# Performance work log

Measured on AMD Instinct MI355X. Metric: run time of the kernel, lower is better.

Reference implementation:

```python
import jax, jax.numpy as jnp
import numpy as np

GAMMA = -0.1   # l0_gamma
ZETA = 1.1     # l0_zeta
BETA = 0.66    # l0_beta (hard-concrete temperature)
LAMBDA = 0.01  # lambda_reg (post-warmup current_lambda)
EPS = 1e-12


def _layernorm(x, g, b, eps=1e-5):
    mu = jnp.mean(x, axis=-1, keepdims=True)
    var = jnp.var(x, axis=-1, keepdims=True)
    return (x - mu) / jnp.sqrt(var + eps) * g + b


def setup_inputs() -> dict:
    key = jax.random.key(0)
    ks = jax.random.split(key, 12)
    B, N, D, H, E, C = 8, 512, 512, 256, 32, 2
    node_feat = jax.random.normal(ks[0], (B, N, D), jnp.float32)
    labels = jax.random.randint(ks[1], (B,), 0, C)
    a = (jax.random.uniform(ks[2], (B, N, N)) < 0.05).astype(jnp.float32)
    adjs = jnp.maximum(a, jnp.swapaxes(a, 1, 2)) * (1.0 - jnp.eye(N, dtype=jnp.float32))
    masks = jnp.ones((B, N), jnp.float32)
    init = lambda k, shp, fan: jax.random.normal(k, shp, jnp.float32) / np.sqrt(fan).astype(np.float32)
    return {
        "node_feat": node_feat, "labels": labels, "adjs": adjs, "masks": masks,
        # edge scorer MLP: concat([h_i,h_j]) -> edge_dim -> 1, factorized as Wa@h_i + Wb@h_j
        "Wa": init(ks[3], (D, E), D), "Wb": init(ks[4], (D, E), D), "be": jnp.zeros((E,), jnp.float32),
        "W2e": init(ks[5], (E, 1), E), "b2e": jnp.zeros((1,), jnp.float32),
        # conv: Linear(feature_dim, hidden_dim)
        "Wconv": init(ks[6], (D, H), D), "bconv": jnp.zeros((H,), jnp.float32),
        # classifier: Linear(H,H//2) -> ReLU -> LayerNorm -> spectral_norm(Linear(H//2,C))
        "W1c": init(ks[7], (H, H // 2), H), "b1c": jnp.zeros((H // 2,), jnp.float32),
        "ln_g": jnp.ones((H // 2,), jnp.float32), "ln_b": jnp.zeros((H // 2,), jnp.float32),
        "W2c": init(ks[8], (H // 2, C), H // 2), "b2c": jnp.zeros((C,), jnp.float32),
        "u_sn": jax.random.normal(ks[9], (C,), jnp.float32),  # spectral-norm power-iteration buffer
    }


def reference(node_feat, labels, adjs, masks, Wa, Wb, be, W2e, b2e,
              Wconv, bconv, W1c, b1c, ln_g, ln_b, W2c, b2c, u_sn):
    B = node_feat.shape[0]
    # F.normalize(node_feat, p=2, dim=2)
    nrm = jnp.sqrt(jnp.sum(node_feat * node_feat, axis=2, keepdims=True))
    nf = node_feat / jnp.maximum(nrm, EPS)
    # edge scoring: logAlpha[b,i,j] = MLP([h_i ; h_j])
    e1 = nf @ Wa                                  # [B,N,E]
    e2 = nf @ Wb                                  # [B,N,E]
    hpair = jax.nn.relu(e1[:, :, None, :] + e2[:, None, :, :] + be)   # [B,N,N,E]
    logAlpha = jnp.einsum('bije,e->bij', hpair, W2e[:, 0]) + b2e[0]    # [B,N,N]
    # deterministic hard-concrete gate (eval mode): clip(sigmoid(logAlpha)*(zeta-gamma)+gamma, 0, 1)
    gate = jnp.clip(jax.nn.sigmoid(logAlpha) * (ZETA - GAMMA) + GAMMA, 0.0, 1.0)
    edge_weights = gate * adjs
    # aggregate: row-normalized weighted adjacency
    wadj = adjs * edge_weights
    row_sum = jnp.sum(wadj, axis=2, keepdims=True) + 1e-8
    h = jnp.einsum('bij,bjd->bid', wadj / row_sum, nf)
    h = jax.nn.relu(h @ Wconv + bconv)            # [B,N,H]
    # edge-weighted attention pooling: node importance = weighted degree, masked softmax
    imp = jnp.sum(wadj, axis=2)                    # [B,N]
    attn_logits = jnp.where(masks > 0, imp, -1e9)
    attn = jax.nn.softmax(attn_logits, axis=1)
    graph_rep = jnp.einsum('bn,bnh->bh', attn, h)  # [B,H]
    # classifier
    z = jax.nn.relu(graph_rep @ W1c + b1c)
    z = _layernorm(z, ln_g, ln_b)
    # spectral norm (1 power iteration, u/v stop-gradded like torch buffers)
    v = W2c @ u_sn
    v = jax.lax.stop_gradient(v / jnp.maximum(jnp.linalg.norm(v), EPS))
    u2 = W2c.T @ v
    u2 = jax.lax.stop_gradient(u2 / jnp.maximum(jnp.linalg.norm(u2), EPS))
    sigma = v @ (W2c @ u2)
    logits = z @ (W2c / sigma) + b2c              # [B,C]
    # losses
    logp = jax.nn.log_softmax(logits, axis=1)
    cls_loss = -jnp.mean(logp[jnp.arange(B), labels])
    l0_penalty = jnp.sum(jax.nn.sigmoid(logAlpha - BETA * jnp.log(-GAMMA / ZETA)))
    total_loss = cls_loss + LAMBDA * l0_penalty
    return logits, total_loss, adjs * edge_weights
```

## Files before the change

### kernel.cpp

```cpp
#include <hip/hip_runtime.h>


#define Bsz 8
#define Nn  512
#define Dd  512
#define Hh  256
#define Ee  32

#define WS_NFPK   0L
#define WS_E1     1048576L
#define WS_E2     1179648L
#define WS_WADJB  1310720L
#define WS_RS     1835008L
#define WS_L0     1839104L
#define WS_HAGGB  1839112L
#define WS_H      2363400L
#define WS_GR     3411976L

typedef __bf16 bf16x8 __attribute__((ext_vector_type(8)));
typedef float  f32x4  __attribute__((ext_vector_type(4)));

__device__ inline ushort f2bf(float f) {
  union { float f; unsigned u; } c; c.f = f;
  return (ushort)((c.u + 0x7fffu + ((c.u >> 16) & 1u)) >> 16);
}

__global__ __launch_bounds__(256) void norm_e12_fused(
    const float* __restrict__ nfeat, const float* __restrict__ Wa,
    const float* __restrict__ Wb, const float* __restrict__ be,
    ushort* __restrict__ nfpk, float* __restrict__ e1, float* __restrict__ e2,
    float* __restrict__ row_sum, float* __restrict__ gr,
    float* __restrict__ l0_sum)
{
  const int blk = blockIdx.x;
  const int r0 = blk*16;
  const int b = r0 >> 9;
  const int t = threadIdx.x;
  const int r = t >> 4;
  const int seg = t & 15;

  __shared__ ushort As[(63*17 + 15 + 1)*8];
  __shared__ ushort Bs[4*64*8];

  float4 v[8];
  const float* src = nfeat + (long)(r0 + r)*Dd + seg*32;
  #pragma unroll
  for (int i = 0; i < 8; ++i) v[i] = *(const float4*)(src + i*4);
  float s = 0.f;
  #pragma unroll
  for (int i = 0; i < 8; ++i)
    s += v[i].x*v[i].x + v[i].y*v[i].y + v[i].z*v[i].z + v[i].w*v[i].w;
  #pragma unroll
  for (int m = 1; m < 16; m <<= 1) s += __shfl_xor(s, m, 16);
  const float sc = 1.f / fmaxf(sqrtf(s), 1e-12f);
  #pragma unroll
  for (int q = 0; q < 4; ++q) {
    ushort tmp[8];
    const float4 a = v[2*q], bq = v[2*q+1];
    tmp[0]=f2bf(a.x*sc);  tmp[1]=f2bf(a.y*sc);  tmp[2]=f2bf(a.z*sc);  tmp[3]=f2bf(a.w*sc);
    tmp[4]=f2bf(bq.x*sc); tmp[5]=f2bf(bq.y*sc); tmp[6]=f2bf(bq.z*sc); tmp[7]=f2bf(bq.w*sc);
    *(uint4*)(As + ((seg*4 + q)*17 + r)*8) = *(uint4*)tmp;
  }
  if (t < 16) row_sum[r0 + t] = 0.f;
  if (blk == 0) {
    for (int p = t; p < Bsz*Hh; p += 256) gr[p] = 0.f;
    if (t == 0) *l0_sum = 0.f;
  }
  __syncthreads();

  #pragma unroll
  for (int p = 0; p < 4; ++p) {
    const int g = t + p*256;
    const int oct = g >> 9, d = g & 511;
    ushort tmp[8];
    #pragma unroll
    for (int j = 0; j < 8; ++j)
      tmp[j] = As[((d >> 3)*17 + oct*8 + j)*8 + (d & 7)];
    const long og = ((r0 & 511) >> 3) + oct;
    *(uint4*)(nfpk + ((long)b*262144 + (og*512 + d)*8)) = *(uint4*)tmp;
  }

  const int lane = t & 63, l15 = lane & 15, quad = lane >> 4;
  const int w = t >> 6;
  f32x4 acc = {0.f, 0.f, 0.f, 0.f};
  const int bn = t & 63, bkq = t >> 6;
  for (int k0 = 0; k0 < 512; k0 += 32) {
    ushort tmp[8];
    {
      const float* W = (bn < 32) ? Wa : Wb;
      const int col = bn & 31;
      #pragma unroll
      for (int j = 0; j < 8; ++j)
        tmp[j] = f2bf(W[(long)(k0 + bkq*8 + j)*Ee + col]);
    }
    __syncthreads();
    *(uint4*)(Bs + (bkq*64 + bn)*8) = *(uint4*)tmp;
    __syncthreads();
    const bf16x8 af  = *(const bf16x8*)(As + (((k0 >> 3) + quad)*17 + l15)*8);
    const bf16x8 bfr = *(const bf16x8*)(Bs + (quad*64 + w*16 + l15)*8);
    acc = __builtin_amdgcn_mfma_f32_16x16x32_bf16(af, bfr, acc, 0, 0, 0);
  }
  const int col = w*16 + l15;
  #pragma unroll
  for (int rr = 0; rr < 4; ++rr) {
    const int row = r0 + quad*4 + rr;
    if (col < 32) e1[(long)row*Ee + col] = acc[rr] + be[col];
    else          e2[(long)row*Ee + (col - 32)] = acc[rr];
  }
}

__global__ __launch_bounds__(256) void edge_kernel(
    const float* __restrict__ e1, const float* __restrict__ e2,
    const float* __restrict__ W2e, const float* __restrict__ b2e,
    const float* __restrict__ adjs, float* __restrict__ out_wadj,
    ushort* __restrict__ wadj_b, float* __restrict__ row_sum,
    float* __restrict__ l0_sum)
{
  const int b  = blockIdx.z;
  const int i0 = blockIdx.y * 32;
  const int j0 = blockIdx.x * 128;
  const int t  = threadIdx.x;

  __shared__ float e2s[32*132];

  #pragma unroll
  for (int itr = 0; itr < 4; ++itr) {
    const int idx = t + itr*256;
    const int kq = idx & 7, jg = idx >> 3;
    const float4 v = *(const float4*)(e2 + ((long)(b*Nn + j0 + jg))*Ee + kq*4);
    e2s[(kq*4+0)*132 + jg] = v.x;
    e2s[(kq*4+1)*132 + jg] = v.y;
    e2s[(kq*4+2)*132 + jg] = v.z;
    e2s[(kq*4+3)*132 + jg] = v.w;
  }

  const int pair  = t >> 4;
  const int jslot = t & 15;
  const int ia = i0 + pair*2;
  const int ib = ia + 1;
  const int ja = jslot*4;
  const int jb = ja + 64;

  float e1af[32], e1bf[32], w2f[32];
  #pragma unroll
  for (int q = 0; q < 8; ++q) {
    *(float4*)(&e1af[q*4]) = *(const float4*)(e1 + ((long)(b*Nn + ia))*Ee + q*4);
    *(float4*)(&e1bf[q*4]) = *(const float4*)(e1 + ((long)(b*Nn + ib))*Ee + q*4);
    *(float4*)(&w2f[q*4])  = *(const float4*)(W2e + q*4);
  }
  const float b2 = b2e[0];
  __syncthreads();

  float acc[2][8] = {};
  #pragma unroll
  for (int k = 0; k < 32; ++k) {
    const float4 va = *(const float4*)(e2s + k*132 + ja);
    const float4 vb = *(const float4*)(e2s + k*132 + jb);
    const float w = w2f[k];
    const float ea = e1af[k], eb = e1bf[k];
    acc[0][0] += fmaxf(ea+va.x, 0.f)*w;
    acc[0][1] += fmaxf(ea+va.y, 0.f)*w;
    acc[0][2] += fmaxf(ea+va.z, 0.f)*w;
    acc[0][3] += fmaxf(ea+va.w, 0.f)*w;
    acc[0][4] += fmaxf(ea+vb.x, 0.f)*w;
    acc[0][5] += fmaxf(ea+vb.y, 0.f)*w;
    acc[0][6] += fmaxf(ea+vb.z, 0.f)*w;
    acc[0][7] += fmaxf(ea+vb.w, 0.f)*w;
    acc[1][0] += fmaxf(eb+va.x, 0.f)*w;
    acc[1][1] += fmaxf(eb+va.y, 0.f)*w;
    acc[1][2] += fmaxf(eb+va.z, 0.f)*w;
    acc[1][3] += fmaxf(eb+va.w, 0.f)*w;
    acc[1][4] += fmaxf(eb+vb.x, 0.f)*w;
    acc[1][5] += fmaxf(eb+vb.y, 0.f)*w;
    acc[1][6] += fmaxf(eb+vb.z, 0.f)*w;
    acc[1][7] += fmaxf(eb+vb.w, 0.f)*w;
  }

  float rs[2] = {0.f, 0.f};
  float l0acc = 0.f;
  #pragma unroll
  for (int ii = 0; ii < 2; ++ii) {
    const int i = (ii == 0) ? ia : ib;
    const float* arow = adjs     + ((long)(b*Nn + i))*Nn + j0;
    ushort* bwrow     = wadj_b   + ((long)(b*Nn + i))*Nn + j0;
    float* outrow     = out_wadj + ((long)(b*Nn + i))*Nn + j0;
    #pragma unroll
    for (int h2 = 0; h2 < 2; ++h2) {
      const int jl = (h2 == 0) ? ja : jb;
      const float4 av = *(const float4*)(arow + jl);
      float wv[4];
      #pragma unroll
      for (int c = 0; c < 4; ++c) {
        const float logA = acc[ii][h2*4 + c] + b2;
        const float sg = 1.f/(1.f + expf(-logA));
        const float gate = fminf(fmaxf(sg*1.2f - 0.1f, 0.f), 1.f);
        const float a = (c==0)?av.x:(c==1)?av.y:(c==2)?av.z:av.w;
        const float w = gate*a*a;
        wv[c] = w;
        rs[ii] += w;
        l0acc += 1.f/(1.f + expf(-(logA + 1.58261088f)));
      }
      ushort4 bw;
      bw.x = f2bf(wv[0]); bw.y = f2bf(wv[1]); bw.z = f2bf(wv[2]); bw.w = f2bf(wv[3]);
      *(ushort4*)(bwrow + jl) = bw;
      outrow[jl+0] = wv[0]; outrow[jl+1] = wv[1];
      outrow[jl+2] = wv[2]; outrow[jl+3] = wv[3];
    }
  }

  #pragma unroll
  for (int m = 1; m < 16; m <<= 1) {
    rs[0] += __shfl_xor(rs[0], m, 16);
    rs[1] += __shfl_xor(rs[1], m, 16);
  }
  if (jslot == 0) {
    atomicAdd(&row_sum[b*Nn + ia], rs[0]);
    atomicAdd(&row_sum[b*Nn + ib], rs[1]);
  }
  #pragma unroll
  for (int m = 1; m < 64; m <<= 1) l0acc += __shfl_xor(l0acc, m, 64);
  if ((t & 63) == 0) atomicAdd(l0_sum, l0acc);
}

template<int OP>
__global__ __launch_bounds__(256) void mfma_gemm64(
    const ushort* __restrict__ A, const ushort* __restrict__ Bpk,
    const float* __restrict__ Bf32, int M, int N, int K,
    long sA, long sB, long sC, const float* __restrict__ aux,
    ushort* __restrict__ Cb, float* __restrict__ Cf)
{
  const int bb = blockIdx.z;
  const int m0 = blockIdx.y*64, n0 = blockIdx.x*64;
  const int t = threadIdx.x;
  const int lane = t & 63, l15 = lane & 15, quad = lane >> 4;
  const int wv = t >> 6, wr = wv & 1, wc = wv >> 1;

  __shared__ ushort As[(3*65 + 63 + 1)*8];
  __shared__ ushort Bs[4*64*8];

  const ushort* Ab = A + (long)bb*sA;
  const int am = t >> 2, akq = t & 3;
  const int bn = t & 63, bkq = t >> 6;

  f32x4 acc[2][2];
  #pragma unroll
  for (int i = 0; i < 2; ++i)
    #pragma unroll
    for (int j = 0; j < 2; ++j) acc[i][j] = (f32x4){0.f,0.f,0.f,0.f};

  uint4 ra = *(const uint4*)(Ab + (long)(m0+am)*K + akq*8);
  uint4 rbu;
  float rbf[8];
  if (OP == 0) {
    const ushort* Bb = Bpk + (long)bb*sB;
    rbu = *(const uint4*)(Bb + ((long)bkq*N + n0 + bn)*8);
  } else {
    #pragma unroll
    for (int j = 0; j < 8; ++j) rbf[j] = Bf32[(long)(bkq*8 + j)*N + n0 + bn];
  }

  for (int k0 = 0; k0 < K; k0 += 32) {
    *(uint4*)(As + (akq*65 + am)*8) = ra;
    if (OP == 0) {
      *(uint4*)(Bs + (bkq*64 + bn)*8) = rbu;
    } else {
      ushort tmp[8];
      #pragma unroll
      for (int j = 0; j < 8; ++j) tmp[j] = f2bf(rbf[j]);
      *(uint4*)(Bs + (bkq*64 + bn)*8) = *(uint4*)tmp;
    }
    __syncthreads();
    if (k0 + 32 < K) {
      ra = *(const uint4*)(Ab + (long)(m0+am)*K + (k0+32) + akq*8);
      if (OP == 0) {
        const ushort* Bb = Bpk + (long)bb*sB;
        rbu = *(const uint4*)(Bb + ((long)(((k0+32) >> 3) + bkq)*N + n0 + bn)*8);
      } else {
        #pragma unroll
        for (int j = 0; j < 8; ++j)
          rbf[j] = Bf32[(long)(k0 + 32 + bkq*8 + j)*N + n0 + bn];
      }
    }
    bf16x8 af[2], bfr[2];
    #pragma unroll
    for (int i = 0; i < 2; ++i)
      af[i] = *(const bf16x8*)(As + (quad*65 + wr*32 + i*16 + l15)*8);
    #pragma unroll
    for (int j = 0; j < 2; ++j)
      bfr[j] = *(const bf16x8*)(Bs + (quad*64 + wc*32 + j*16 + l15)*8);
    #pragma unroll
    for (int i = 0; i < 2; ++i)
      #pragma unroll
      for (int j = 0; j < 2; ++j)
        acc[i][j] = __builtin_amdgcn_mfma_f32_16x16x32_bf16(
            af[i], bfr[j], acc[i][j], 0, 0, 0);
    __syncthreads();
  }

  #pragma unroll
  for (int i = 0; i < 2; ++i) {
    #pragma unroll
    for (int j = 0; j < 2; ++j) {
      const int col = n0 + wc*32 + j*16 + l15;
      #pragma unroll
      for (int rr = 0; rr < 4; ++rr) {
        const int row = m0 + wr*32 + i*16 + quad*4 + rr;
        float v2 = acc[i][j][rr];
        if (OP == 0) {
          const float scl = 1.f/(aux[bb*M + row] + 1e-8f);
          Cb[(long)bb*sC + (long)row*N + col] = f2bf(v2*scl);
        } else {
          v2 += aux[col];
          Cf[(long)row*N + col] = fmaxf(v2, 0.f);
        }
      }
    }
  }
}

__global__ __launch_bounds__(256) void pool_fused(
    const float* __restrict__ row_sum, const float* __restrict__ masks,
    const float* __restrict__ h, float* __restrict__ gr)
{
  const int ic = blockIdx.x, b = blockIdx.y;
  const int t = threadIdx.x;
  __shared__ float red[256];
  __shared__ float attn_s[64];
  const float m0 = masks[b*Nn + t], m1 = masks[b*Nn + t + 256];
  const float l0v = (m0 > 0.f) ? row_sum[b*Nn + t] : -1e9f;
  const float l1v = (m1 > 0.f) ? row_sum[b*Nn + t + 256] : -1e9f;
  red[t] = fmaxf(l0v, l1v); __syncthreads();
  for (int s = 128; s > 0; s >>= 1) { if (t < s) red[t] = fmaxf(red[t], red[t+s]); __syncthreads(); }
  const float mx = red[0]; __syncthreads();
  const float ev0 = expf(l0v - mx), ev1 = expf(l1v - mx);
  red[t] = ev0 + ev1; __syncthreads();
  for (int s = 128; s > 0; s >>= 1) { if (t < s) red[t] += red[t+s]; __syncthreads(); }
  const float sinv = 1.f/red[0];
  __syncthreads();
  if (t < 64) {
    const int node = ic*64 + t;
    const float mm = masks[b*Nn + node];
    const float lv = (mm > 0.f) ? row_sum[b*Nn + node] : -1e9f;
    attn_s[t] = expf(lv - mx)*sinv;
  }
  __syncthreads();
  float acc = 0.f;
  #pragma unroll 4
  for (int i2 = 0; i2 < 64; ++i2)
    acc += attn_s[i2]*h[((long)(b*Nn + ic*64 + i2))*Hh + t];
  atomicAdd(&gr[b*Hh + t], acc);
}

__global__ __launch_bounds__(256) void classifier_kernel(
    const float* __restrict__ gr, const float* __restrict__ W1c,
    const float* __restrict__ b1c, const float* __restrict__ ln_g,
    const float* __restrict__ ln_b, const float* __restrict__ W2c,
    const float* __restrict__ b2c, const float* __restrict__ u_sn,
    const int* __restrict__ labels, const float* __restrict__ l0_sum,
    float* __restrict__ out)
{
  const int t = threadIdx.x;
  __shared__ float grs[2048];
  __shared__ float z[8][128];
  __shared__ float red[256];
  __shared__ float vv[128];
  __shared__ float mu_s[8], ri_s[8];
  __shared__ float lg[16];
  for (int p = t; p < 2048; p += 256) grs[p] = gr[p];
  __syncthreads();
  #pragma unroll
  for (int p = 0; p < 4; ++p) {
    const int idx = t + p*256;
    const int b = idx >> 7, o = idx & 127;
    float acc = b1c[o];
    for (int d = 0; d < 256; ++d) acc += grs[b*256 + d]*W1c[d*128 + o];
    z[b][o] = fmaxf(acc, 0.f);
  }
  __syncthreads();
  if (t < 8) {
    float mu = 0.f;
    for (int o = 0; o < 128; ++o) mu += z[t][o];
    mu *= (1.f/128.f);
    float var = 0.f;
    for (int o = 0; o < 128; ++o) { const float d = z[t][o]-mu; var += d*d; }
    var *= (1.f/128.f);
    mu_s[t] = mu; ri_s[t] = rsqrtf(var + 1e-5f);
  }
  const float u0 = u_sn[0], u1 = u_sn[1];
  float vt = 0.f;
  if (t < 128) { vt = W2c[2*t]*u0 + W2c[2*t+1]*u1; vv[t] = vt; }
  red[t] = (t < 128) ? vt*vt : 0.f;
  __syncthreads();
  for (int s = 128; s > 0; s >>= 1) { if (t < s) red[t] += red[t+s]; __syncthreads(); }
  const float vninv = 1.f/fmaxf(sqrtf(red[0]), 1e-12f);
  __syncthreads();
  red[t] = (t < 128) ? W2c[2*t]*vv[t]*vninv : 0.f;
  __syncthreads();
  for (int s = 128; s > 0; s >>= 1) { if (t < s) red[t] += red[t+s]; __syncthreads(); }
  const float u20 = red[0];
  __syncthreads();
  red[t] = (t < 128) ? W2c[2*t+1]*vv[t]*vninv : 0.f;
  __syncthreads();
  for (int s = 128; s > 0; s >>= 1) { if (t < s) red[t] += red[t+s]; __syncthreads(); }
  const float u21 = red[0];
  __syncthreads();
  const float uninv = 1.f/fmaxf(sqrtf(u20*u20 + u21*u21), 1e-12f);
  const float u2n0 = u20*uninv, u2n1 = u21*uninv;
  red[t] = (t < 128) ? vv[t]*vninv*(W2c[2*t]*u2n0 + W2c[2*t+1]*u2n1) : 0.f;
  __syncthreads();
  for (int s = 128; s > 0; s >>= 1) { if (t < s) red[t] += red[t+s]; __syncthreads(); }
  const float sinv = 1.f/red[0];
  __syncthreads();
  if (t < 16) {
    const int b = t >> 1, c = t & 1;
    const float mu = mu_s[b], ri = ri_s[b];
    float acc = 0.f;
    for (int o = 0; o < 128; ++o) {
      const float zln = (z[b][o]-mu)*ri*ln_g[o] + ln_b[o];
      acc += zln*W2c[2*o + c];
    }
    const float lgv = acc*sinv + b2c[c];
    lg[t] = lgv;
    out[t] = lgv;
  }
  __syncthreads();
  if (t == 0) {
    float closs = 0.f;
    for (int b = 0; b < 8; ++b) {
      const float a0 = lg[2*b], a1 = lg[2*b+1];
      const float m = fmaxf(a0, a1);
      const float lse = m + logf(expf(a0-m) + expf(a1-m));
      closs += lse - lg[2*b + labels[b]];
    }
    closs *= (1.f/8.f);
    out[16] = closs + 0.01f*l0_sum[0];
  }
}

extern "C" void kernel_launch(void* const* d_in, const int* in_sizes, int n_in,
                              void* d_out, int out_size, void* d_ws, size_t ws_size,
                              hipStream_t stream) {
  const float* node_feat = (const float*)d_in[0];
  const int*   labels    = (const int*)d_in[1];
  const float* adjs      = (const float*)d_in[2];
  const float* masks     = (const float*)d_in[3];
  const float* Wa        = (const float*)d_in[4];
  const float* Wb        = (const float*)d_in[5];
  const float* be        = (const float*)d_in[6];
  const float* W2e       = (const float*)d_in[7];
  const float* b2e       = (const float*)d_in[8];
  const float* Wconv     = (const float*)d_in[9];
  const float* bconv     = (const float*)d_in[10];
  const float* W1c       = (const float*)d_in[11];
  const float* b1c       = (const float*)d_in[12];
  const float* ln_g      = (const float*)d_in[13];
  const float* ln_b      = (const float*)d_in[14];
  const float* W2c       = (const float*)d_in[15];
  const float* b2c       = (const float*)d_in[16];
  const float* u_sn      = (const float*)d_in[17];

  float* out = (float*)d_out;
  float* ws  = (float*)d_ws;
  ushort* nfpk   = (ushort*)(ws + WS_NFPK);
  float*  e1     = ws + WS_E1;
  float*  e2     = ws + WS_E2;
  ushort* wadjb  = (ushort*)(ws + WS_WADJB);
  float*  row_sum= ws + WS_RS;
  float*  l0s    = ws + WS_L0;
  ushort* haggb  = (ushort*)(ws + WS_HAGGB);
  float*  h      = ws + WS_H;
  float*  gr     = ws + WS_GR;

  norm_e12_fused<<<256, 256, 0, stream>>>(node_feat, Wa, Wb, be, nfpk, e1, e2,
                                          row_sum, gr, l0s);
  edge_kernel<<<dim3(Nn/128, Nn/32, Bsz), 256, 0, stream>>>(
      e1, e2, W2e, b2e, adjs, out + 17, wadjb, row_sum, l0s);
  mfma_gemm64<0><<<dim3(8, 8, 8), 256, 0, stream>>>(
      wadjb, nfpk, nullptr, 512, 512, 512, 262144L, 262144L, 262144L,
      row_sum, haggb, nullptr);
  mfma_gemm64<1><<<dim3(4, 64, 1), 256, 0, stream>>>(
      haggb, nullptr, Wconv, 4096, 256, 512, 0, 0, 0,
      bconv, nullptr, h);
  pool_fused<<<dim3(8, Bsz), 256, 0, stream>>>(row_sum, masks, h, gr);
  classifier_kernel<<<1, 256, 0, stream>>>(gr, W1c, b1c, ln_g, ln_b, W2c, b2c,
                                           u_sn, labels, l0s, out);
}
```

Measured before the change: 201.8 us.

## Reassociate conv GEMM before aggregation and fuse aggregation with attention pooling

```diff
diff --git a/kernel.cpp b/kernel.cpp
--- a/kernel.cpp
+++ b/kernel.cpp
@@ -7,15 +7,15 @@
 #define Hh  256
 #define Ee  32
 
-#define WS_NFPK   0L
-#define WS_E1     1048576L
-#define WS_E2     1179648L
-#define WS_WADJB  1310720L
+#define WS_NFCPK  0L
+#define WS_E1     524288L
+#define WS_E2     655360L
+#define WS_WADJB  786432L
 #define WS_RS     1835008L
 #define WS_L0     1839104L
-#define WS_HAGGB  1839112L
-#define WS_H      2363400L
-#define WS_GR     3411976L
+#define WS_GR     1839112L
+#define WS_WABPK  1841160L
+#define WS_WCPK   1857544L
 
 typedef __bf16 bf16x8 __attribute__((ext_vector_type(8)));
 typedef float  f32x4  __attribute__((ext_vector_type(4)));
@@ -25,10 +25,34 @@
   return (ushort)((c.u + 0x7fffu + ((c.u >> 16) & 1u)) >> 16);
 }
 
-__global__ __launch_bounds__(256) void norm_e12_fused(
-    const float* __restrict__ nfeat, const float* __restrict__ Wa,
-    const float* __restrict__ Wb, const float* __restrict__ be,
-    ushort* __restrict__ nfpk, float* __restrict__ e1, float* __restrict__ e2,
+__global__ __launch_bounds__(256) void pack_weights(
+    const float* __restrict__ Wconv, const float* __restrict__ Wa,
+    const float* __restrict__ Wb, ushort* __restrict__ wcpk,
+    ushort* __restrict__ wabpk)
+{
+  const int g = blockIdx.x*256 + threadIdx.x;
+  if (g < 16384) {
+    const int kq = g >> 8, n = g & 255;
+    ushort tmp[8];
+    #pragma unroll
+    for (int j = 0; j < 8; ++j) tmp[j] = f2bf(Wconv[(kq*8 + j)*Hh + n]);
+    *(uint4*)(wcpk + (long)g*8) = *(uint4*)tmp;
+  } else if (g < 16384 + 4096) {
+    const int gg = g - 16384;
+    const int kq = gg >> 6, n = gg & 63;
+    const float* W = (n < 32) ? Wa : Wb;
+    const int e = n & 31;
+    ushort tmp[8];
+    #pragma unroll
+    for (int j = 0; j < 8; ++j) tmp[j] = f2bf(W[(kq*8 + j)*Ee + e]);
+    *(uint4*)(wabpk + (long)gg*8) = *(uint4*)tmp;
+  }
+}
+
+__global__ __launch_bounds__(256) void norm_e12_nfc(
+    const float* __restrict__ nfeat, const ushort* __restrict__ wabpk,
+    const ushort* __restrict__ wcpk, const float* __restrict__ be,
+    ushort* __restrict__ nfcpk, float* __restrict__ e1, float* __restrict__ e2,
     float* __restrict__ row_sum, float* __restrict__ gr,
     float* __restrict__ l0_sum)
 {
@@ -40,7 +64,8 @@
   const int seg = t & 15;
 
   __shared__ ushort As[(63*17 + 15 + 1)*8];
-  __shared__ ushort Bs[4*64*8];
+  __shared__ ushort BsA[4*64*8];
+  __shared__ ushort BsC[4*256*8];
 
   float4 v[8];
   const float* src = nfeat + (long)(r0 + r)*Dd + seg*32;
@@ -66,46 +91,82 @@
     for (int p = t; p < Bsz*Hh; p += 256) gr[p] = 0.f;
     if (t == 0) *l0_sum = 0.f;
   }
-  __syncthreads();
-
+
+  const int lane = t & 63, l15 = lane & 15, quad = lane >> 4;
+  const int w = t >> 6;
+  const int abq = t >> 6, abn = t & 63;
+
+  f32x4 acc_e = {0.f, 0.f, 0.f, 0.f};
+  f32x4 acc_c[4];
+  #pragma unroll
+  for (int j = 0; j < 4; ++j) acc_c[j] = (f32x4){0.f,0.f,0.f,0.f};
+
+  uint4 pab = *(const uint4*)(wabpk + ((long)abq*64 + abn)*8);
+  uint4 pc[4];
   #pragma unroll
   for (int p = 0; p < 4; ++p) {
     const int g = t + p*256;
-    const int oct = g >> 9, d = g & 511;
+    pc[p] = *(const uint4*)(wcpk + ((long)(g >> 8)*256 + (g & 255))*8);
+  }
+  __syncthreads();
+
+  for (int k0 = 0; k0 < 512; k0 += 32) {
+    if (k0 > 0) __syncthreads();
+    *(uint4*)(BsA + (abq*64 + abn)*8) = pab;
+    #pragma unroll
+    for (int p = 0; p < 4; ++p) {
+      const int g = t + p*256;
+      *(uint4*)(BsC + ((g >> 8)*256 + (g & 255))*8) = pc[p];
+    }
+    __syncthreads();
+    if (k0 + 32 < 512) {
+      const int kb = (k0 + 32) >> 3;
+      pab = *(const uint4*)(wabpk + ((long)(kb + abq)*64 + abn)*8);
+      #pragma unroll
+      for (int p = 0; p < 4; ++p) {
+        const int g = t + p*256;
+        pc[p] = *(const uint4*)(wcpk + ((long)(kb + (g >> 8))*256 + (g & 255))*8);
+      }
+    }
+    const bf16x8 af = *(const bf16x8*)(As + (((k0 >> 3) + quad)*17 + l15)*8);
+    const bf16x8 bfa = *(const bf16x8*)(BsA + (quad*64 + w*16 + l15)*8);
+    acc_e = __builtin_amdgcn_mfma_f32_16x16x32_bf16(af, bfa, acc_e, 0, 0, 0);
+    #pragma unroll
+    for (int fn = 0; fn < 4; ++fn) {
+      const bf16x8 bfc = *(const bf16x8*)(BsC + (quad*256 + w*64 + fn*16 + l15)*8);
+      acc_c[fn] = __builtin_amdgcn_mfma_f32_16x16x32_bf16(af, bfc, acc_c[fn], 0, 0, 0);
+    }
+  }
+
+  {
+    const int col = w*16 + l15;
+    #pragma unroll
+    for (int rr = 0; rr < 4; ++rr) {
+      const int row = r0 + quad*4 + rr;
+      if (col < 32) e1[(long)row*Ee + col] = acc_e[rr] + be[col];
+      else          e2[(long)row*Ee + (col - 32)] = acc_e[rr];
+    }
+  }
+
+  __syncthreads();
+  ushort* tile = BsC;
+  #pragma unroll
+  for (int fn = 0; fn < 4; ++fn) {
+    const int col = w*64 + fn*16 + l15;
+    #pragma unroll
+    for (int rr = 0; rr < 4; ++rr)
+      tile[(quad*4 + rr)*260 + col] = f2bf(acc_c[fn][rr]);
+  }
+  __syncthreads();
+  #pragma unroll
+  for (int p = 0; p < 2; ++p) {
+    const int g = t + p*256;
+    const int oct = g >> 8, c = g & 255;
     ushort tmp[8];
     #pragma unroll
-    for (int j = 0; j < 8; ++j)
-      tmp[j] = As[((d >> 3)*17 + oct*8 + j)*8 + (d & 7)];
+    for (int j = 0; j < 8; ++j) tmp[j] = tile[(oct*8 + j)*260 + c];
     const long og = ((r0 & 511) >> 3) + oct;
-    *(uint4*)(nfpk + ((long)b*262144 + (og*512 + d)*8)) = *(uint4*)tmp;
-  }
-
-  const int lane = t & 63, l15 = lane & 15, quad = lane >> 4;
-  const int w = t >> 6;
-  f32x4 acc = {0.f, 0.f, 0.f, 0.f};
-  const int bn = t & 63, bkq = t >> 6;
-  for (int k0 = 0; k0 < 512; k0 += 32) {
-    ushort tmp[8];
-    {
-      const float* W = (bn < 32) ? Wa : Wb;
-      const int col = bn & 31;
-      #pragma unroll
-      for (int j = 0; j < 8; ++j)
-        tmp[j] = f2bf(W[(long)(k0 + bkq*8 + j)*Ee + col]);
-    }
-    __syncthreads();
-    *(uint4*)(Bs + (bkq*64 + bn)*8) = *(uint4*)tmp;
-    __syncthreads();
-    const bf16x8 af  = *(const bf16x8*)(As + (((k0 >> 3) + quad)*17 + l15)*8);
-    const bf16x8 bfr = *(const bf16x8*)(Bs + (quad*64 + w*16 + l15)*8);
-    acc = __builtin_amdgcn_mfma_f32_16x16x32_bf16(af, bfr, acc, 0, 0, 0);
-  }
-  const int col = w*16 + l15;
-  #pragma unroll
-  for (int rr = 0; rr < 4; ++rr) {
-    const int row = r0 + quad*4 + rr;
-    if (col < 32) e1[(long)row*Ee + col] = acc[rr] + be[col];
-    else          e2[(long)row*Ee + (col - 32)] = acc[rr];
+    *(uint4*)(nfcpk + ((long)b*16384 + og*256 + c)*8) = *(uint4*)tmp;
   }
 }
 
@@ -222,12 +283,10 @@
   if ((t & 63) == 0) atomicAdd(l0_sum, l0acc);
 }
 
-template<int OP>
-__global__ __launch_bounds__(256) void mfma_gemm64(
-    const ushort* __restrict__ A, const ushort* __restrict__ Bpk,
-    const float* __restrict__ Bf32, int M, int N, int K,
-    long sA, long sB, long sC, const float* __restrict__ aux,
-    ushort* __restrict__ Cb, float* __restrict__ Cf)
+__global__ __launch_bounds__(256) void gemm_pool(
+    const ushort* __restrict__ wadjb, const ushort* __restrict__ nfcpk,
+    const float* __restrict__ row_sum, const float* __restrict__ masks,
+    const float* __restrict__ bconv, float* __restrict__ gr)
 {
   const int bb = blockIdx.z;
   const int m0 = blockIdx.y*64, n0 = blockIdx.x*64;
@@ -237,8 +296,13 @@
 
   __shared__ ushort As[(3*65 + 63 + 1)*8];
   __shared__ ushort Bs[4*64*8];
-
-  const ushort* Ab = A + (long)bb*sA;
+  __shared__ float ptile[64*65];
+  __shared__ float red[256];
+  __shared__ float attn_s[64];
+  __shared__ float mx_s, sinv_s;
+
+  const ushort* Ab = wadjb + (long)bb*262144;
+  const ushort* Bb = nfcpk + (long)bb*131072;
   const int am = t >> 2, akq = t & 3;
   const int bn = t & 63, bkq = t >> 6;
 
@@ -248,38 +312,17 @@
     #pragma unroll
     for (int j = 0; j < 2; ++j) acc[i][j] = (f32x4){0.f,0.f,0.f,0.f};
 
-  uint4 ra = *(const uint4*)(Ab + (long)(m0+am)*K + akq*8);
-  uint4 rbu;
-  float rbf[8];
-  if (OP == 0) {
-    const ushort* Bb = Bpk + (long)bb*sB;
-    rbu = *(const uint4*)(Bb + ((long)bkq*N + n0 + bn)*8);
-  } else {
-    #pragma unroll
-    for (int j = 0; j < 8; ++j) rbf[j] = Bf32[(long)(bkq*8 + j)*N + n0 + bn];
-  }
-
-  for (int k0 = 0; k0 < K; k0 += 32) {
+  uint4 ra = *(const uint4*)(Ab + (long)(m0+am)*512 + akq*8);
+  uint4 rb = *(const uint4*)(Bb + ((long)bkq*256 + n0 + bn)*8);
+
+  for (int k0 = 0; k0 < 512; k0 += 32) {
+    if (k0 > 0) __syncthreads();
     *(uint4*)(As + (akq*65 + am)*8) = ra;
-    if (OP == 0) {
-      *(uint4*)(Bs + (bkq*64 + bn)*8) = rbu;
-    } else {
-      ushort tmp[8];
-      #pragma unroll
-      for (int j = 0; j < 8; ++j) tmp[j] = f2bf(rbf[j]);
-      *(uint4*)(Bs + (bkq*64 + bn)*8) = *(uint4*)tmp;
-    }
+    *(uint4*)(Bs + (bkq*64 + bn)*8) = rb;
     __syncthreads();
-    if (k0 + 32 < K) {
-      ra = *(const uint4*)(Ab + (long)(m0+am)*K + (k0+32) + akq*8);
-      if (OP == 0) {
-        const ushort* Bb = Bpk + (long)bb*sB;
-        rbu = *(const uint4*)(Bb + ((long)(((k0+32) >> 3) + bkq)*N + n0 + bn)*8);
-      } else {
-        #pragma unroll
-        for (int j = 0; j < 8; ++j)
-          rbf[j] = Bf32[(long)(k0 + 32 + bkq*8 + j)*N + n0 + bn];
-      }
+    if (k0 + 32 < 512) {
+      ra = *(const uint4*)(Ab + (long)(m0+am)*512 + (k0+32) + akq*8);
+      rb = *(const uint4*)(Bb + ((long)(((k0+32) >> 3) + bkq)*256 + n0 + bn)*8);
     }
     bf16x8 af[2], bfr[2];
     #pragma unroll
@@ -294,61 +337,54 @@
       for (int j = 0; j < 2; ++j)
         acc[i][j] = __builtin_amdgcn_mfma_f32_16x16x32_bf16(
             af[i], bfr[j], acc[i][j], 0, 0, 0);
+  }
+  __syncthreads();
+
+  {
+    const float mk0 = masks[bb*Nn + t], mk1 = masks[bb*Nn + t + 256];
+    const float lv0 = (mk0 > 0.f) ? row_sum[bb*Nn + t] : -1e9f;
+    const float lv1 = (mk1 > 0.f) ? row_sum[bb*Nn + t + 256] : -1e9f;
+    red[t] = fmaxf(lv0, lv1); __syncthreads();
+    for (int s = 128; s > 0; s >>= 1) { if (t < s) red[t] = fmaxf(red[t], red[t+s]); __syncthreads(); }
+    if (t == 0) mx_s = red[0];
     __syncthreads();
+    const float mx = mx_s;
+    red[t] = expf(lv0 - mx) + expf(lv1 - mx); __syncthreads();
+    for (int s = 128; s > 0; s >>= 1) { if (t < s) red[t] += red[t+s]; __syncthreads(); }
+    if (t == 0) sinv_s = 1.f/red[0];
+    __syncthreads();
+    if (t < 64) {
+      const int node = m0 + t;
+      const float mm = masks[bb*Nn + node];
+      const float lv = (mm > 0.f) ? row_sum[bb*Nn + node] : -1e9f;
+      attn_s[t] = expf(lv - mx)*sinv_s;
+    }
+    __syncthreads();
   }
 
   #pragma unroll
   for (int i = 0; i < 2; ++i) {
     #pragma unroll
     for (int j = 0; j < 2; ++j) {
-      const int col = n0 + wc*32 + j*16 + l15;
+      const int lcol = wc*32 + j*16 + l15;
+      const float bias = bconv[n0 + lcol];
       #pragma unroll
       for (int rr = 0; rr < 4; ++rr) {
-        const int row = m0 + wr*32 + i*16 + quad*4 + rr;
-        float v2 = acc[i][j][rr];
-        if (OP == 0) {
-          const float scl = 1.f/(aux[bb*M + row] + 1e-8f);
-          Cb[(long)bb*sC + (long)row*N + col] = f2bf(v2*scl);
-        } else {
-          v2 += aux[col];
-          Cf[(long)row*N + col] = fmaxf(v2, 0.f);
-        }
+        const int lrow = wr*32 + i*16 + quad*4 + rr;
+        const int row = m0 + lrow;
+        const float scl = 1.f/(row_sum[bb*Nn + row] + 1e-8f);
+        const float hv = fmaxf(acc[i][j][rr]*scl + bias, 0.f);
+        ptile[lrow*65 + lcol] = hv * attn_s[lrow];
       }
     }
   }
-}
-
-__global__ __launch_bounds__(256) void pool_fused(
-    const float* __restrict__ row_sum, const float* __restrict__ masks,
-    const float* __restrict__ h, float* __restrict__ gr)
-{
-  const int ic = blockIdx.x, b = blockIdx.y;
-  const int t = threadIdx.x;
-  __shared__ float red[256];
-  __shared__ float attn_s[64];
-  const float m0 = masks[b*Nn + t], m1 = masks[b*Nn + t + 256];
-  const float l0v = (m0 > 0.f) ? row_sum[b*Nn + t] : -1e9f;
-  const float l1v = (m1 > 0.f) ? row_sum[b*Nn + t + 256] : -1e9f;
-  red[t] = fmaxf(l0v, l1v); __syncthreads();
-  for (int s = 128; s > 0; s >>= 1) { if (t < s) red[t] = fmaxf(red[t], red[t+s]); __syncthreads(); }
-  const float mx = red[0]; __syncthreads();
-  const float ev0 = expf(l0v - mx), ev1 = expf(l1v - mx);
-  red[t] = ev0 + ev1; __syncthreads();
-  for (int s = 128; s > 0; s >>= 1) { if (t < s) red[t] += red[t+s]; __syncthreads(); }
-  const float sinv = 1.f/red[0];
   __syncthreads();
   if (t < 64) {
-    const int node = ic*64 + t;
-    const float mm = masks[b*Nn + node];
-    const float lv = (mm > 0.f) ? row_sum[b*Nn + node] : -1e9f;
-    attn_s[t] = expf(lv - mx)*sinv;
-  }
-  __syncthreads();
-  float acc = 0.f;
-  #pragma unroll 4
-  for (int i2 = 0; i2 < 64; ++i2)
-    acc += attn_s[i2]*h[((long)(b*Nn + ic*64 + i2))*Hh + t];
-  atomicAdd(&gr[b*Hh + t], acc);
+    float s = 0.f;
+    #pragma unroll 4
+    for (int rr = 0; rr < 64; ++rr) s += ptile[rr*65 + t];
+    atomicAdd(&gr[bb*Hh + n0 + t], s);
+  }
 }
 
 __global__ __launch_bounds__(256) void classifier_kernel(
@@ -461,27 +497,23 @@
 
   float* out = (float*)d_out;
   float* ws  = (float*)d_ws;
-  ushort* nfpk   = (ushort*)(ws + WS_NFPK);
+  ushort* nfcpk  = (ushort*)(ws + WS_NFCPK);
   float*  e1     = ws + WS_E1;
   float*  e2     = ws + WS_E2;
   ushort* wadjb  = (ushort*)(ws + WS_WADJB);
   float*  row_sum= ws + WS_RS;
   float*  l0s    = ws + WS_L0;
-  ushort* haggb  = (ushort*)(ws + WS_HAGGB);
-  float*  h      = ws + WS_H;
   float*  gr     = ws + WS_GR;
-
-  norm_e12_fused<<<256, 256, 0, stream>>>(node_feat, Wa, Wb, be, nfpk, e1, e2,
-                                          row_sum, gr, l0s);
+  ushort* wabpk  = (ushort*)(ws + WS_WABPK);
+  ushort* wcpk   = (ushort*)(ws + WS_WCPK);
+
+  pack_weights<<<80, 256, 0, stream>>>(Wconv, Wa, Wb, wcpk, wabpk);
+  norm_e12_nfc<<<256, 256, 0, stream>>>(node_feat, wabpk, wcpk, be, nfcpk,
+                                        e1, e2, row_sum, gr, l0s);
   edge_kernel<<<dim3(Nn/128, Nn/32, Bsz), 256, 0, stream>>>(
       e1, e2, W2e, b2e, adjs, out + 17, wadjb, row_sum, l0s);
-  mfma_gemm64<0><<<dim3(8, 8, 8), 256, 0, stream>>>(
-      wadjb, nfpk, nullptr, 512, 512, 512, 262144L, 262144L, 262144L,
-      row_sum, haggb, nullptr);
-  mfma_gemm64<1><<<dim3(4, 64, 1), 256, 0, stream>>>(
-      haggb, nullptr, Wconv, 4096, 256, 512, 0, 0, 0,
-      bconv, nullptr, h);
-  pool_fused<<<dim3(8, Bsz), 256, 0, stream>>>(row_sum, masks, h, gr);
+  gemm_pool<<<dim3(Hh/64, Nn/64, Bsz), 256, 0, stream>>>(
+      wadjb, nfcpk, row_sum, masks, bconv, gr);
   classifier_kernel<<<1, 256, 0, stream>>>(gr, W1c, b1c, ln_g, ln_b, W2c, b2c,
                                            u_sn, labels, l0s, out);
 }
```

After: 199.9 us. No clear change (-0.9%).
